# Performance work log

Hardware: AMD Instinct MI355X
Metric: run time of the kernel (lower is better)

## Reference

```python
import jax, jax.numpy as jnp
import numpy as np

N, NFEAT, NHID, NCLASS, NHEADS = 4096, 512, 64, 40, 8
ALPHA = 0.2
NEG = -9e15


def setup_inputs() -> dict:
    key = jax.random.key(0)
    ks = jax.random.split(key, 6)
    x = jax.random.normal(ks[0], (N, NFEAT), dtype=jnp.float32)
    adj = jax.random.randint(ks[1], (2, N, N), 0, 2, dtype=jnp.int32)
    # Xavier-ish scaled params
    W1 = jax.random.normal(ks[2], (NHEADS, NFEAT, NHID), dtype=jnp.float32) * (1.0 / np.sqrt(NFEAT))
    a1 = jax.random.normal(ks[3], (NHEADS, 2, NHID), dtype=jnp.float32) * (1.0 / np.sqrt(2 * NHID))
    Wo = jax.random.normal(ks[4], (NHEADS * NHID, NCLASS), dtype=jnp.float32) * (1.0 / np.sqrt(NHEADS * NHID))
    ao = jax.random.normal(ks[5], (2, NCLASS), dtype=jnp.float32) * (1.0 / np.sqrt(2 * NCLASS))
    return {"x": x, "adj": adj, "W1": W1, "a1": a1, "Wo": Wo, "ao": ao}


def _gat_layer(h, adj_mask, W, a_src, a_dst, concat):
    # h: [N,F]; W: [...,F,F']; a_src/a_dst: [...,F']
    if W.ndim == 3:  # multi-head: [H,F,F']
        Wh = jnp.einsum('nf,hfd->hnd', h, W)              # [H,N,F']
        f1 = jnp.einsum('hnd,hd->hn', Wh, a_src)           # [H,N]
        f2 = jnp.einsum('hnd,hd->hn', Wh, a_dst)
        e = jax.nn.leaky_relu(f1[:, :, None] + f2[:, None, :], ALPHA)  # [H,N,N]
        e = jnp.where(adj_mask[None], e, NEG)
        att = jax.nn.softmax(e, axis=-1)
        out = jnp.einsum('hnm,hmd->hnd', att, Wh)          # [H,N,F']
    else:
        Wh = h @ W                                         # [N,F']
        f1 = Wh @ a_src
        f2 = Wh @ a_dst
        e = jax.nn.leaky_relu(f1[:, None] + f2[None, :], ALPHA)
        e = jnp.where(adj_mask, e, NEG)
        att = jax.nn.softmax(e, axis=-1)
        out = att @ Wh
    return jax.nn.elu(out) if concat else out


def reference(x, adj, W1, a1, Wo, ao):
    adj1 = adj[1] > 0
    adj0 = adj[0] > 0
    # layer 1: NHEADS heads, concat=True
    h = _gat_layer(x, adj1, W1, a1[:, 0], a1[:, 1], concat=True)   # [H,N,NHID]
    h = jnp.transpose(h, (1, 0, 2)).reshape(x.shape[0], -1)        # [N, H*NHID]
    # output layer: concat=False, then outer ELU + log_softmax
    out = _gat_layer(h, adj0, Wo, ao[0], ao[1], concat=False)      # [N, NCLASS]
    out = jax.nn.elu(out)
    return jax.nn.log_softmax(out, axis=1)
```

## Files before the change

kernel.cpp:

```cpp
#include <hip/hip_runtime.h>
#include <hip/hip_bf16.h>

#define N      4096
#define NFEAT  512
#define NHID   64
#define NHEADS 8
#define NCLASS 40
#define ALPHA  0.2f
#define LOG2E  1.44269504f

typedef unsigned short u16;
typedef unsigned int   u32;
typedef __attribute__((ext_vector_type(8))) short bf16x8;
typedef __attribute__((ext_vector_type(4))) float f32x4;

__device__ __forceinline__ float b2f(u16 u) {
    return __uint_as_float(((u32)u) << 16);
}
__device__ __forceinline__ u32 rnd_hi(float f) {
    u32 u = __float_as_uint(f);
    return u + 0x7FFFu + ((u >> 16) & 1u);
}
__device__ __forceinline__ u32 pk2(float lo, float hi) {
    __hip_bfloat162 h = __float22bfloat162_rn(make_float2(lo, hi));
    return *(u32*)&h;
}
__device__ __forceinline__ u16 f2b(float f) {
    return (u16)(rnd_hi(f) >> 16);
}
__device__ __forceinline__ float mexp(int m, float t) {
    return m ? __builtin_amdgcn_exp2f(fmaxf(t, ALPHA * t)) : 0.f;
}
__device__ __forceinline__ bf16x8 ones_frag() {
    union { u16 u[8]; bf16x8 v; } o;
    #pragma unroll
    for (int j = 0; j < 8; ++j) o.u[j] = 0x3F80;
    return o.v;
}
__device__ __forceinline__ void gload_lds16(const u16* g, u16* l) {
    __builtin_amdgcn_global_load_lds(
        (const __attribute__((address_space(1))) void*)g,
        (__attribute__((address_space(3))) void*)l,
        16, 0, 0);
}

__global__ __launch_bounds__(256) void kcx(const float* __restrict__ x,
                                           u16* __restrict__ xb) {
    const int g = blockIdx.x * 256 + threadIdx.x;
    const size_t base = (size_t)g * 8;
    float4 v0 = *(const float4*)&x[base];
    float4 v1 = *(const float4*)&x[base + 4];
    uint4 o;
    o.x = pk2(v0.x, v0.y); o.y = pk2(v0.z, v0.w);
    o.z = pk2(v1.x, v1.y); o.w = pk2(v1.z, v1.w);
    *(uint4*)&xb[base] = o;
}

__global__ __launch_bounds__(256) void kcw(const float* __restrict__ W1,
                                           u16* __restrict__ W1b) {
    __shared__ float ts[64 * 68];
    const int t  = threadIdx.x;
    const int f0 = blockIdx.x * 64;
    const int h  = blockIdx.y;
    #pragma unroll
    for (int i = 0; i < 4; ++i) {
        int flat = t + 256 * i;
        int row = flat >> 4;
        int c4  = (flat & 15) * 4;
        *(float4*)&ts[row * 68 + c4] =
            *(const float4*)&W1[((size_t)h * 512 + f0 + row) * 64 + c4];
    }
    __syncthreads();
    const int d  = t >> 2;
    const int fs = (t & 3) * 16;
    u32 p[8];
    #pragma unroll
    for (int j = 0; j < 8; ++j)
        p[j] = pk2(ts[(fs + 2 * j) * 68 + d], ts[(fs + 2 * j + 1) * 68 + d]);
    u32* dst = (u32*)&W1b[((size_t)(h * 64 + d)) * 512 + f0 + fs];
    *(uint4*)dst       = make_uint4(p[0], p[1], p[2], p[3]);
    *(uint4*)(dst + 4) = make_uint4(p[4], p[5], p[6], p[7]);
}

__global__ __launch_bounds__(256, 4) void k1m_gemm1(const u16* __restrict__ xb,
                                                    const u16* __restrict__ W1b,
                                                    const float* __restrict__ a1,
                                                    u16* __restrict__ Wh1T,
                                                    float* __restrict__ F1,
                                                    float* __restrict__ F2) {
    __shared__ u16 xs[64 * 72];
    __shared__ u16 wvs[64 * 72];
    const int t    = threadIdx.x;
    const int n0   = blockIdx.x * 64;
    const int h    = blockIdx.y;
    const int lane = t & 63;
    const int l15  = lane & 15;
    const int q    = lane >> 4;
    const int wrow = (t >> 6) * 16;
    f32x4 acc[4];
    #pragma unroll
    for (int df = 0; df < 4; ++df)
        #pragma unroll
        for (int r = 0; r < 4; ++r) acc[df][r] = 0.f;
    for (int f0 = 0; f0 < 512; f0 += 64) {
        uint4 sx[2], sw[2];
        #pragma unroll
        for (int i = 0; i < 2; ++i) {
            int flat = t + 256 * i;
            int row = flat >> 3;
            int c8  = (flat & 7) * 8;
            sx[i] = *(const uint4*)&xb[(size_t)(n0 + row) * 512 + f0 + c8];
            sw[i] = *(const uint4*)&W1b[((size_t)(h * 64 + row)) * 512 + f0 + c8];
        }
        __syncthreads();
        #pragma unroll
        for (int i = 0; i < 2; ++i) {
            int flat = t + 256 * i;
            int row = flat >> 3;
            int c8  = (flat & 7) * 8;
            *(uint4*)&xs[row * 72 + c8]  = sx[i];
            *(uint4*)&wvs[row * 72 + c8] = sw[i];
        }
        __syncthreads();
        #pragma unroll
        for (int ks = 0; ks < 2; ++ks) {
            int k0 = ks * 32 + q * 8;
            bf16x8 a = *(const bf16x8*)&xs[(wrow + l15) * 72 + k0];
            #pragma unroll
            for (int df = 0; df < 4; ++df) {
                bf16x8 b = *(const bf16x8*)&wvs[(df * 16 + l15) * 72 + k0];
                acc[df] = __builtin_amdgcn_mfma_f32_16x16x32_bf16(a, b, acc[df], 0, 0, 0);
            }
        }
    }
    #pragma unroll
    for (int df = 0; df < 4; ++df) {
        uint2 o;
        o.x = pk2(acc[df][0], acc[df][1]);
        o.y = pk2(acc[df][2], acc[df][3]);
        *(uint2*)&Wh1T[((size_t)(h * 64 + df * 16 + l15)) * 4096 + n0 + wrow + q * 4] = o;
    }
    float a1v[4], a2v[4];
    #pragma unroll
    for (int df = 0; df < 4; ++df) {
        a1v[df] = a1[h * 128 + df * 16 + l15];
        a2v[df] = a1[h * 128 + 64 + df * 16 + l15];
    }
    #pragma unroll
    for (int r = 0; r < 4; ++r) {
        float s1 = 0.f, s2 = 0.f;
        #pragma unroll
        for (int df = 0; df < 4; ++df) {
            s1 += acc[df][r] * a1v[df];
            s2 += acc[df][r] * a2v[df];
        }
        #pragma unroll
        for (int off = 8; off >= 1; off >>= 1) {
            s1 += __shfl_xor(s1, off);
            s2 += __shfl_xor(s2, off);
        }
        if (l15 == 0) {
            int n = n0 + wrow + q * 4 + r;
            F1[h * 4096 + n] = s1 * LOG2E;
            F2[h * 4096 + n] = s2 * LOG2E;
        }
    }
}

__global__ __launch_bounds__(256, 4) void k3_attn1(const int* __restrict__ adj1,
                                                   const u16* __restrict__ Wh1T,
                                                   const float* __restrict__ F1,
                                                   const float* __restrict__ F2,
                                                   float* __restrict__ h1) {
    __shared__ __align__(16) u16 wbf[32 * 136];
    __shared__ __align__(16) u16 whT[64 * 128];
    __shared__ float f1s[32];
    __shared__ float zs[32];
    const int t     = threadIdx.x;
    const int n0    = blockIdx.x * 32;
    const int h     = blockIdx.y;
    const int lane  = t & 63;
    const int l15   = lane & 15;
    const int q     = lane >> 4;
    const int wv    = t >> 6;
    const int rb    = (wv & 1) * 16;
    const int dh    = wv >> 1;
    const int c4    = (t & 31) * 4;
    const int rg    = t >> 5;
    const bf16x8 bones = ones_frag();
    if (t < 32) f1s[t] = F1[h * N + n0 + t];

    const int lsub = lane >> 4;
    const int slot = lane & 15;
    const u16* gsrc[4];
    #pragma unroll
    for (int i = 0; i < 4; ++i) {
        int row_l = wv * 16 + i * 4 + lsub;
        int sc    = (slot ^ ((i * 4 + lsub) & 7)) * 8;
        gsrc[i] = Wh1T + ((size_t)(h * 64 + row_l)) * 4096 + sc;
    }
    u16* ldst = &whT[wv * 2048];
    const int xb7 = l15 & 7;

    f32x4 accd[2], accz;
    #pragma unroll
    for (int j = 0; j < 2; ++j)
        #pragma unroll
        for (int r = 0; r < 4; ++r) accd[j][r] = 0.f;
    #pragma unroll
    for (int r = 0; r < 4; ++r) accz[r] = 0.f;

    int4 aprev[4];
    #pragma unroll
    for (int i = 0; i < 4; ++i)
        aprev[i] = *(const int4*)&adj1[(size_t)(n0 + rg + 8 * i) * N + c4];
    float4 f2n = *(const float4*)&F2[h * N + c4];
    __syncthreads();

    for (int m0 = 0; m0 < 4096; m0 += 128) {
        #pragma unroll
        for (int i = 0; i < 4; ++i)
            gload_lds16(gsrc[i] + m0, ldst + i * 512);
        const float4 F2v = f2n;
        const int mn = (m0 + 128 < 4096) ? m0 + 128 : 0;
        f2n = *(const float4*)&F2[h * N + mn + c4];
        #pragma unroll
        for (int i = 0; i < 4; ++i) {
            const int rr = rg + 8 * i;
            int4 a4 = aprev[i];
            aprev[i] = *(const int4*)&adj1[(size_t)(n0 + rr) * N + mn + c4];
            float f1v = f1s[rr];
            float w0 = mexp(a4.x, f1v + F2v.x);
            float w1 = mexp(a4.y, f1v + F2v.y);
            float w2 = mexp(a4.z, f1v + F2v.z);
            float w3 = mexp(a4.w, f1v + F2v.w);
            uint2 pk;
            pk.x = pk2(w0, w1);
            pk.y = pk2(w2, w3);
            *(uint2*)&wbf[rr * 136 + c4] = pk;
        }
        __syncthreads();
        #pragma unroll
        for (int ks = 0; ks < 4; ++ks) {
            int k0 = ks * 32 + q * 8;
            bf16x8 a = *(const bf16x8*)&wbf[(rb + l15) * 136 + k0];
            #pragma unroll
            for (int j = 0; j < 2; ++j) {
                const int df = dh * 2 + j;
                bf16x8 b = *(const bf16x8*)
                    &whT[(df * 16 + l15) * 128 + (((ks * 4 + q) ^ xb7) * 8)];
                accd[j] = __builtin_amdgcn_mfma_f32_16x16x32_bf16(a, b, accd[j], 0, 0, 0);
            }
            if (dh == 0)
                accz = __builtin_amdgcn_mfma_f32_16x16x32_bf16(a, bones, accz, 0, 0, 0);
        }
        __syncthreads();
    }
    if (dh == 0 && l15 == 0) {
        #pragma unroll
        for (int r = 0; r < 4; ++r) zs[rb + q * 4 + r] = accz[r];
    }
    __syncthreads();
    #pragma unroll
    for (int r = 0; r < 4; ++r) {
        const int nl = rb + q * 4 + r;
        const float z = fmaxf(zs[nl], 1e-30f);
        #pragma unroll
        for (int j = 0; j < 2; ++j) {
            float v = accd[j][r] / z;
            v = v > 0.f ? v : __expf(v) - 1.f;
            h1[(size_t)(n0 + nl) * 512 + h * 64 + (dh * 2 + j) * 16 + l15] = v;
        }
    }
}

__global__ __launch_bounds__(256) void k4_gemm2(const float* __restrict__ h1,
                                                const float* __restrict__ Wo,
                                                const float* __restrict__ ao,
                                                float* __restrict__ F1o,
                                                float* __restrict__ F2o,
                                                u16* __restrict__ Wh2T) {
    const int t = threadIdx.x;
    const int c = t & 63;
    const int n = blockIdx.x * 4 + (t >> 6);
    float acc = 0.f;
    if (c < NCLASS) {
        const float* hrow = &h1[(size_t)n * 512];
        #pragma unroll 8
        for (int f = 0; f < 512; ++f)
            acc += hrow[f] * Wo[f * NCLASS + c];
        Wh2T[(size_t)c * 4096 + n] = f2b(acc);
    }
    float s1 = (c < NCLASS) ? acc * ao[c] : 0.f;
    float s2 = (c < NCLASS) ? acc * ao[NCLASS + c] : 0.f;
    #pragma unroll
    for (int off = 32; off >= 1; off >>= 1) {
        s1 += __shfl_xor(s1, off);
        s2 += __shfl_xor(s2, off);
    }
    if (c == 0) {
        F1o[n] = s1 * LOG2E;
        F2o[n] = s2 * LOG2E;
    }
}

__global__ __launch_bounds__(256, 5) void k5a_attn2(const int* __restrict__ adj0,
                                                    const u16* __restrict__ Wh2T,
                                                    const float* __restrict__ F1o,
                                                    const float* __restrict__ F2o,
                                                    float* __restrict__ pacc,
                                                    float* __restrict__ pz) {
    __shared__ __align__(16) u16 wbf[64 * 136];
    __shared__ __align__(16) u16 whT[48 * 128];
    __shared__ float f1s[64];
    const int t     = threadIdx.x;
    const int n0    = blockIdx.x * 64;
    const int chunk = blockIdx.y;
    const int mbase = chunk * 256;
    const int lane  = t & 63;
    const int l15   = lane & 15;
    const int q     = lane >> 4;
    const int wrow  = (t >> 6) * 16;
    const int c4    = (t & 31) * 4;
    const int rg    = t >> 5;
    const bf16x8 bones = ones_frag();
    if (t < 64) f1s[t] = F1o[n0 + t];
    #pragma unroll
    for (int i = 0; i < 4; ++i)
        whT[40 * 128 + t + 256 * i] = 0;

    const int wv   = t >> 6;
    const int lsub = lane >> 4;
    const int slot = lane & 15;
    const int ninst = (wv < 2) ? 4 : ((wv == 2) ? 2 : 0);
    const u16* gsrc[4];
    #pragma unroll
    for (int i = 0; i < 4; ++i) {
        int row_l = wv * 16 + i * 4 + lsub;
        int rl    = (row_l < 40) ? row_l : 0;
        int sc    = (slot ^ ((i * 4 + lsub) & 7)) * 8;
        gsrc[i] = Wh2T + (size_t)rl * 4096 + sc;
    }
    u16* ldst = &whT[wv * 2048];
    const int xb7 = l15 & 7;

    f32x4 acc[4];
    #pragma unroll
    for (int df = 0; df < 4; ++df)
        #pragma unroll
        for (int r = 0; r < 4; ++r) acc[df][r] = 0.f;

    int4 aprev[8];
    #pragma unroll
    for (int i = 0; i < 8; ++i)
        aprev[i] = *(const int4*)&adj0[(size_t)(n0 + rg + 8 * i) * N + mbase + c4];
    __syncthreads();

    #pragma unroll
    for (int mt = 0; mt < 2; ++mt) {
        const int m0 = mbase + mt * 128;
        #pragma unroll
        for (int i = 0; i < 4; ++i)
            if (i < ninst)
                gload_lds16(gsrc[i] + m0, ldst + i * 512);
        float4 F2v = *(const float4*)&F2o[m0 + c4];
        #pragma unroll
        for (int i = 0; i < 8; ++i) {
            int rr = rg + 8 * i;
            int4 a4 = aprev[i];
            float f1v = f1s[rr];
            float w0 = mexp(a4.x, f1v + F2v.x);
            float w1 = mexp(a4.y, f1v + F2v.y);
            float w2 = mexp(a4.z, f1v + F2v.z);
            float w3 = mexp(a4.w, f1v + F2v.w);
            uint2 pk;
            pk.x = pk2(w0, w1);
            pk.y = pk2(w2, w3);
            *(uint2*)&wbf[rr * 136 + c4] = pk;
        }
        int mn = mbase + ((mt + 1) & 1) * 128;
        #pragma unroll
        for (int i = 0; i < 8; ++i)
            aprev[i] = *(const int4*)&adj0[(size_t)(n0 + rg + 8 * i) * N + mn + c4];
        __syncthreads();
        #pragma unroll
        for (int ks = 0; ks < 4; ++ks) {
            int k0 = ks * 32 + q * 8;
            bf16x8 a = *(const bf16x8*)&wbf[(wrow + l15) * 136 + k0];
            #pragma unroll
            for (int df = 0; df < 3; ++df) {
                bf16x8 b = *(const bf16x8*)
                    &whT[(df * 16 + l15) * 128 + (((ks * 4 + q) ^ xb7) * 8)];
                acc[df] = __builtin_amdgcn_mfma_f32_16x16x32_bf16(a, b, acc[df], 0, 0, 0);
            }
            acc[3] = __builtin_amdgcn_mfma_f32_16x16x32_bf16(a, bones, acc[3], 0, 0, 0);
        }
        __syncthreads();
    }
    #pragma unroll
    for (int r = 0; r < 4; ++r) {
        int n = n0 + wrow + q * 4 + r;
        if (l15 == 0) pz[(size_t)chunk * N + n] = acc[3][r];
        #pragma unroll
        for (int df = 0; df < 3; ++df) {
            int c = df * 16 + l15;
            if (c < NCLASS)
                pacc[((size_t)chunk * N + n) * NCLASS + c] = acc[df][r];
        }
    }
}

__global__ __launch_bounds__(256) void k5b_final(const float* __restrict__ pacc,
                                                 const float* __restrict__ pz,
                                                 float* __restrict__ out) {
    const int t = threadIdx.x;
    const int lane = t & 63;
    const int n = blockIdx.x * 4 + (t >> 6);
    float s = 0.f, Z = 0.f;
    #pragma unroll
    for (int ch = 0; ch < 16; ++ch) {
        Z += pz[(size_t)ch * N + n];
        if (lane < NCLASS) s += pacc[(size_t)(ch * N + n) * NCLASS + lane];
    }
    float v;
    if (lane < NCLASS) {
        v = s / fmaxf(Z, 1e-30f);
        v = v > 0.f ? v : __expf(v) - 1.f;
    } else {
        v = -INFINITY;
    }
    float mx = v;
    #pragma unroll
    for (int off = 32; off >= 1; off >>= 1) mx = fmaxf(mx, __shfl_xor(mx, off));
    float ex = (lane < NCLASS) ? __expf(v - mx) : 0.f;
    #pragma unroll
    for (int off = 32; off >= 1; off >>= 1) ex += __shfl_xor(ex, off);
    float lse = mx + __logf(ex);
    if (lane < NCLASS) out[(size_t)n * NCLASS + lane] = v - lse;
}

extern "C" void kernel_launch(void* const* d_in, const int* in_sizes, int n_in,
                              void* d_out, int out_size, void* d_ws, size_t ws_size,
                              hipStream_t stream) {
    const float* x   = (const float*)d_in[0];
    const int*   adj = (const int*)d_in[1];
    const float* W1  = (const float*)d_in[2];
    const float* a1  = (const float*)d_in[3];
    const float* Wo  = (const float*)d_in[4];
    const float* ao  = (const float*)d_in[5];

    float* ws    = (float*)d_ws;
    float* h1    = ws;
    float* F1    = h1 + 2097152;
    float* F2    = F1 + 32768;
    float* F1o   = F2 + 32768;
    float* F2o   = F1o + 4096;
    float* pz    = F2o + 4096;
    float* pz1   = pz + 65536;
    u16*   Wh1T  = (u16*)(pz1 + 65536);
    u16*   Wh2T  = Wh1T + 2097152;
    float* R     = (float*)(Wh2T + 163840);
    u16*   xb    = (u16*)R;
    u16*   W1b   = xb + 2097152;
    float* pacc  = R;

    const int* adj0 = adj;
    const int* adj1 = adj + (size_t)N * N;

    hipLaunchKernelGGL(kcx,       dim3(1024),   dim3(256), 0, stream, x, xb);
    hipLaunchKernelGGL(kcw,       dim3(8, 8),   dim3(256), 0, stream, W1, W1b);
    hipLaunchKernelGGL(k1m_gemm1, dim3(64, 8),  dim3(256), 0, stream, xb, W1b, a1, Wh1T, F1, F2);
    hipLaunchKernelGGL(k3_attn1,  dim3(128, 8), dim3(256), 0, stream, adj1, Wh1T, F1, F2, h1);
    hipLaunchKernelGGL(k4_gemm2,  dim3(1024),   dim3(256), 0, stream, h1, Wo, ao, F1o, F2o, Wh2T);
    hipLaunchKernelGGL(k5a_attn2, dim3(64, 16), dim3(256), 0, stream, adj0, Wh2T, F1o, F2o, pacc, pz);
    hipLaunchKernelGGL(k5b_final, dim3(1024),   dim3(256), 0, stream, pacc, pz, (float*)d_out);
}
```

Baseline: 318.7 us.

## Double-buffer GEMM1 tiles with direct global-to-LDS loads and XOR swizzle

Rewrites the first-layer projection GEMM main loop to load x and W1 tiles straight into two LDS buffers with global-to-LDS DMA, so the next K-slice loads while MFMAs run on the current one. The padded 72-stride layout is replaced with an unpadded 64-stride layout using an XOR swizzle to avoid bank conflicts. This removes the register staging round-trip and one of the two barriers per tile. In exchange it doubles LDS use per block, which may lower occupancy, and it relies on the gload_lds16 helper and a correct swizzle.

After: 307.7 us. 3.4% less time.

```diff
diff --git a/kernel.cpp b/kernel.cpp
--- a/kernel.cpp
+++ b/kernel.cpp
@@ -88,51 +88,72 @@
                                                     u16* __restrict__ Wh1T,
                                                     float* __restrict__ F1,
                                                     float* __restrict__ F2) {
-    __shared__ u16 xs[64 * 72];
-    __shared__ u16 wvs[64 * 72];
+    __shared__ __align__(16) u16 xs[2][64 * 64];
+    __shared__ __align__(16) u16 wvs[2][64 * 64];
     const int t    = threadIdx.x;
     const int n0   = blockIdx.x * 64;
     const int h    = blockIdx.y;
     const int lane = t & 63;
     const int l15  = lane & 15;
     const int q    = lane >> 4;
-    const int wrow = (t >> 6) * 16;
+    const int wv   = t >> 6;
+    const int wrow = wv * 16;
+    const int lsub = lane >> 3;
+    const int slot = lane & 7;
+    const int xb7  = l15 & 7;
+
+    const u16* gx[2];
+    const u16* gw[2];
+    #pragma unroll
+    for (int i = 0; i < 2; ++i) {
+        const int r  = wv * 16 + i * 8 + lsub;
+        const int sc = (slot ^ lsub) * 8;
+        gx[i] = xb  + (size_t)(n0 + r) * 512 + sc;
+        gw[i] = W1b + ((size_t)(h * 64 + r)) * 512 + sc;
+    }
+
     f32x4 acc[4];
     #pragma unroll
     for (int df = 0; df < 4; ++df)
         #pragma unroll
         for (int r = 0; r < 4; ++r) acc[df][r] = 0.f;
-    for (int f0 = 0; f0 < 512; f0 += 64) {
-        uint4 sx[2], sw[2];
-        #pragma unroll
-        for (int i = 0; i < 2; ++i) {
-            int flat = t + 256 * i;
-            int row = flat >> 3;
-            int c8  = (flat & 7) * 8;
-            sx[i] = *(const uint4*)&xb[(size_t)(n0 + row) * 512 + f0 + c8];
-            sw[i] = *(const uint4*)&W1b[((size_t)(h * 64 + row)) * 512 + f0 + c8];
-        }
-        __syncthreads();
-        #pragma unroll
-        for (int i = 0; i < 2; ++i) {
-            int flat = t + 256 * i;
-            int row = flat >> 3;
-            int c8  = (flat & 7) * 8;
-            *(uint4*)&xs[row * 72 + c8]  = sx[i];
-            *(uint4*)&wvs[row * 72 + c8] = sw[i];
-        }
-        __syncthreads();
-        #pragma unroll
-        for (int ks = 0; ks < 2; ++ks) {
-            int k0 = ks * 32 + q * 8;
-            bf16x8 a = *(const bf16x8*)&xs[(wrow + l15) * 72 + k0];
-            #pragma unroll
-            for (int df = 0; df < 4; ++df) {
-                bf16x8 b = *(const bf16x8*)&wvs[(df * 16 + l15) * 72 + k0];
-                acc[df] = __builtin_amdgcn_mfma_f32_16x16x32_bf16(a, b, acc[df], 0, 0, 0);
-            }
-        }
-    }
+
+#define K1_DMA(P, F0)                                                          \
+    {                                                                          \
+        _Pragma("unroll")                                                      \
+        for (int i = 0; i < 2; ++i) {                                          \
+            gload_lds16(gx[i] + (F0), &xs[P][(wv * 16 + i * 8) * 64]);         \
+            gload_lds16(gw[i] + (F0), &wvs[P][(wv * 16 + i * 8) * 64]);        \
+        }                                                                      \
+    }
+#define K1_MFMA(P)                                                             \
+    {                                                                          \
+        _Pragma("unroll")                                                      \
+        for (int ks = 0; ks < 2; ++ks) {                                       \
+            const int sl = ((ks * 4 + q) ^ xb7) * 8;                           \
+            bf16x8 a = *(const bf16x8*)&xs[P][(wrow + l15) * 64 + sl];         \
+            _Pragma("unroll")                                                  \
+            for (int df = 0; df < 4; ++df) {                                   \
+                bf16x8 b = *(const bf16x8*)&wvs[P][(df * 16 + l15) * 64 + sl]; \
+                acc[df] = __builtin_amdgcn_mfma_f32_16x16x32_bf16(a, b, acc[df], 0, 0, 0); \
+            }                                                                  \
+        }                                                                      \
+    }
+
+    K1_DMA(0, 0)
+    __syncthreads();
+    for (int f0 = 0; f0 < 512; f0 += 128) {
+        K1_DMA(1, f0 + 64)
+        K1_MFMA(0)
+        __syncthreads();
+        if (f0 + 128 < 512)
+            K1_DMA(0, f0 + 128)
+        K1_MFMA(1)
+        __syncthreads();
+    }
+#undef K1_DMA
+#undef K1_MFMA
+
     #pragma unroll
     for (int df = 0; df < 4; ++df) {
         uint2 o;
```
